# Optimization experiments

Hardware: AMD Instinct MI355X
Metric: run time of the kernel (lower is better)

The kernel has to match this reference:

```python
import jax, jax.numpy as jnp
import numpy as np

# ActivationWithGain: activation scaled so a standard-normal input keeps unit variance.
_s = np.random.default_rng(0).standard_normal(1 << 20).astype(np.float32)
GAIN = float(1.0 / (_s / (1.0 + np.exp(-_s))).std())  # SiLU gain ~ 1.787
INV_SQRT2 = np.float32(1.0 / np.sqrt(2.0))


def _act(x):
    return jax.nn.silu(x) * jnp.float32(GAIN)


def setup_inputs() -> dict:
    key = jax.random.key(0)
    ks = jax.random.split(key, 9)
    n_up, n_dn, n_nuc, dim, edim = 512, 512, 256, 256, 32
    n_el = n_up + n_dn
    n_edges = n_el * n_nuc  # dense electron-nucleus bipartite graph
    return {
        "elec_emb": jax.random.normal(ks[0], (n_el, dim), jnp.float32),
        "up_inp": jax.random.normal(ks[1], (n_nuc, dim), jnp.float32),
        "down_inp": jax.random.normal(ks[2], (n_nuc, dim), jnp.float32),
        "edge_emb": jax.random.normal(ks[3], (n_edges, edim), jnp.float32),
        "contr": jax.random.uniform(ks[4], (n_edges,), jnp.float32),
        "norm": jax.random.uniform(ks[5], (n_el,), jnp.float32),
        "W_out": jax.random.normal(ks[6], (dim, dim), jnp.float32) / np.float32(np.sqrt(dim)),
        "b_out": jnp.zeros((dim,), jnp.float32),
        "W_edge": jax.random.normal(ks[7], (edim, dim), jnp.float32) / np.float32(np.sqrt(edim)),
        "W_out2": jax.random.normal(ks[8], (dim, dim), jnp.float32) / np.float32(np.sqrt(dim)),
        "b_out2": jnp.zeros((dim,), jnp.float32),
        "scale1": jnp.ones((), jnp.float32),  # FixedScalingFactor (frozen after init)
        "scale2": jnp.ones((), jnp.float32),
        "n_up": n_up,
        "n_down": n_dn,
        "n_nuclei": n_nuc,
    }


def reference(elec_emb, up_inp, down_inp, edge_emb, contr, norm,
              W_out, b_out, W_edge, W_out2, b_out2, scale1, scale2,
              n_up, n_down, n_nuclei):
    n_el = n_up + n_down
    # adj_idx for a single graph: dense bipartite edges, sorted by electron index
    e_n_i = jnp.repeat(jnp.arange(n_el), n_nuclei)   # [E] electron index per edge
    e_n_k = jnp.tile(jnp.arange(n_nuclei), n_el)     # [E] nucleus index per edge

    out_emb = elec_emb @ W_out + b_out               # Dense(out_dim)

    mask = jnp.arange(n_el) < n_up                   # spin_mask: True for spin-up electrons
    e_n_mask = mask[e_n_i]
    # gather nuclear embeddings per edge, selecting up/down table by electron spin
    inp = jnp.where(e_n_mask[:, None], up_inp[e_n_k], down_inp[e_n_k])  # [E, D]

    weights = edge_emb @ W_edge                      # Dense_no_bias(out_dim), [E, D]
    # FixedScalingFactor: contr only weights the init-time variance estimate;
    # at runtime the op is x * scale1.
    to_elec = inp * weights * scale1                 # [E, D]

    agg = jax.ops.segment_sum(to_elec, e_n_i, num_segments=n_el,
                              indices_are_sorted=True)  # [n_el, D]
    out_emb = (out_emb + agg * norm[:, None]) * scale2
    out_emb = _act(out_emb)
    out_emb = _act(out_emb @ W_out2 + b_out2)
    # residual: shapes match, so rescaled sum
    return (elec_emb + out_emb) * INV_SQRT2
```

## Files before the change

kernel.cpp:

```cpp
#include <hip/hip_runtime.h>
#include <hip/hip_bf16.h>

#define N_EL   1024
#define N_UP   512
#define NNUC   256
#define DIM    256
#define EDIM   32
#define KTOT   8192
#define NKP    16

#define GAIN_F      1.7872135f
#define INV_SQRT2_F 0.7071067811865476f

typedef __attribute__((ext_vector_type(8))) short bf16x8;
typedef __attribute__((ext_vector_type(4))) short bf16x4;
typedef __attribute__((ext_vector_type(4))) float f32x4;

__device__ __forceinline__ short f2bf(float x) {
    union { __hip_bfloat16 h; short s; } u;
    u.h = __float2bfloat16(x);
    return u.s;
}

__global__ __launch_bounds__(256) void prep_kernel(
    const float* __restrict__ up, const float* __restrict__ dn,
    const float* __restrict__ wedge,
    const float* __restrict__ w1, const float* __restrict__ w2,
    const float* __restrict__ elec,
    short* __restrict__ w1f, short* __restrict__ w2f,
    short* __restrict__ elecb, short* __restrict__ Tf)
{
    const int idx = (blockIdx.x << 8) + threadIdx.x;

    if (idx < 65536) {
        {
            const int b  = idx & 7;
            const int l  = (idx >> 3) & 63;
            const int q  = (idx >> 9) & 7;
            const int nt = idx >> 12;
            const int j  = (q << 5) + ((l >> 4) << 3) + b;
            const int d  = (nt << 4) + (l & 15);
            w1f[idx] = f2bf(w1[j * DIM + d]);
            w2f[idx] = f2bf(w2[j * DIM + d]);
        }
        {
            const f32x4 v = *(const f32x4*)(elec + (idx << 2));
            bf16x4 o;
            o[0] = f2bf(v[0]); o[1] = f2bf(v[1]);
            o[2] = f2bf(v[2]); o[3] = f2bf(v[3]);
            *(bf16x4*)(elecb + (idx << 2)) = o;
        }
    }

    {
        const int s   = idx >> 18;
        const int rem = idx & 262143;
        const int kt  = rem >> 10;
        const int dt  = (rem >> 6) & 15;
        const int l   = rem & 63;
        const int d   = (dt << 4) + (l & 15);
        const int jb  = (l >> 4) << 3;
        const float* __restrict__ inp = s ? dn : up;
        const float iv = inp[kt * DIM + d];
        const float* __restrict__ wcol = wedge + d;
        bf16x8 o;
        #pragma unroll
        for (int b = 0; b < 8; ++b)
            o[b] = f2bf(iv * wcol[(jb + b) * DIM]);
        *(bf16x8*)(Tf + ((size_t)s << 21) + ((size_t)rem << 3)) = o;
    }
}

__global__ __launch_bounds__(512) void edge_gemm(
    const float* __restrict__ eemb,
    const short* __restrict__ Tf,
    float* __restrict__ P)
{
    __shared__ short A_lds[2][4096];

    const int tid  = threadIdx.x;
    const int w    = tid >> 6;
    const int lane = tid & 63;
    const int g    = lane >> 4;
    const int c    = lane & 15;
    const int kp   = blockIdx.x & 15;
    const int rt   = blockIdx.x >> 4;
    const int rb   = rt << 5;
    const int kb   = kp << 9;

    const short* __restrict__ Tb = Tf + ((rb < N_UP) ? 0 : (1 << 21));

    const int f  = w;
    const int r_ = f >> 2;
    const int q_ = f & 3;
    const float* __restrict__ Asrc = eemb
        + (size_t)(rb + (r_ << 4) + c) * KTOT
        + kb + (q_ << 5) + (g << 3);

    f32x4 s_lo, s_hi;
    bf16x8 bA[8], bB[8];

    auto STAGE_LOAD = [&](int sub) {
        const float* p = Asrc + (sub << 7);
        s_lo = *(const f32x4*)p;
        s_hi = *(const f32x4*)(p + 4);
    };
    auto STAGE_WRITE = [&](int buf) {
        union { bf16x8 v; short s[8]; } o;
        o.s[0] = f2bf(s_lo[0]); o.s[1] = f2bf(s_lo[1]);
        o.s[2] = f2bf(s_lo[2]); o.s[3] = f2bf(s_lo[3]);
        o.s[4] = f2bf(s_hi[0]); o.s[5] = f2bf(s_hi[1]);
        o.s[6] = f2bf(s_hi[2]); o.s[7] = f2bf(s_hi[3]);
        *(bf16x8*)(&A_lds[buf][(f << 9) + (lane << 3)]) = o.v;
    };
    auto LOADB = [&](int sub, bf16x8 (&bd)[8]) {
        #pragma unroll
        for (int t = 0; t < 2; ++t) {
            const int ct = (w << 1) + t;
            #pragma unroll
            for (int q = 0; q < 4; ++q) {
                const int ktg = (kp << 4) + (sub << 2) + q;
                bd[(t << 2) + q] = *(const bf16x8*)(
                    Tb + (((((ktg << 4) + ct) << 6) + lane) << 3));
            }
        }
    };

    f32x4 acc[2][2] = {{{0.f,0.f,0.f,0.f},{0.f,0.f,0.f,0.f}},
                       {{0.f,0.f,0.f,0.f},{0.f,0.f,0.f,0.f}}};

    auto COMPUTE = [&](int buf, bf16x8 (&bc)[8]) {
        bf16x8 a[2][4];
        #pragma unroll
        for (int rr = 0; rr < 2; ++rr)
            #pragma unroll
            for (int q = 0; q < 4; ++q)
                a[rr][q] = *(const bf16x8*)(
                    &A_lds[buf][((((rr << 2) + q)) << 9) + (lane << 3)]);
        #pragma unroll
        for (int q = 0; q < 4; ++q) {
            acc[0][0] = __builtin_amdgcn_mfma_f32_16x16x32_bf16(a[0][q], bc[q],     acc[0][0], 0, 0, 0);
            acc[0][1] = __builtin_amdgcn_mfma_f32_16x16x32_bf16(a[0][q], bc[4 + q], acc[0][1], 0, 0, 0);
            acc[1][0] = __builtin_amdgcn_mfma_f32_16x16x32_bf16(a[1][q], bc[q],     acc[1][0], 0, 0, 0);
            acc[1][1] = __builtin_amdgcn_mfma_f32_16x16x32_bf16(a[1][q], bc[4 + q], acc[1][1], 0, 0, 0);
        }
    };

    STAGE_LOAD(0);
    LOADB(0, bA);
    STAGE_WRITE(0);
    __syncthreads();

    #pragma unroll
    for (int sub = 0; sub < 4; ++sub) {
        if ((sub & 1) == 0) {
            if (sub < 3) { STAGE_LOAD(sub + 1); LOADB(sub + 1, bB); }
            COMPUTE(0, bA);
        } else {
            if (sub < 3) { STAGE_LOAD(sub + 1); LOADB(sub + 1, bA); }
            COMPUTE(1, bB);
        }
        if (sub < 3) STAGE_WRITE((sub & 1) ^ 1);
        __syncthreads();
    }

    float* __restrict__ Pp = P + ((size_t)kp << 18);
    #pragma unroll
    for (int rr = 0; rr < 2; ++rr)
        #pragma unroll
        for (int t = 0; t < 2; ++t) {
            const int ct = (w << 1) + t;
            #pragma unroll
            for (int j = 0; j < 4; ++j) {
                const int row = rb + (rr << 4) + (g << 2) + j;
                Pp[(row << 8) + (ct << 4) + c] = acc[rr][t][j];
            }
        }
}

__global__ __launch_bounds__(256) void reduce_kernel(
    const float* __restrict__ P,
    const float* __restrict__ s1p,
    float* __restrict__ agg)
{
    const int idx = (blockIdx.x << 8) + threadIdx.x;
    const float s1 = *s1p;
    f32x4 s = {0.f, 0.f, 0.f, 0.f};
    #pragma unroll
    for (int kp = 0; kp < NKP; ++kp) {
        const f32x4 v = *(const f32x4*)(P + ((size_t)kp << 18) + (idx << 2));
        s[0] += v[0]; s[1] += v[1]; s[2] += v[2]; s[3] += v[3];
    }
    s[0] *= s1; s[1] *= s1; s[2] *= s1; s[3] *= s1;
    *(f32x4*)(agg + (idx << 2)) = s;
}

__global__ __launch_bounds__(512) void out_kernel(
    const short* __restrict__ elecb,
    const short* __restrict__ w1f, const short* __restrict__ w2f,
    const float* __restrict__ elec, const float* __restrict__ agg,
    const float* __restrict__ norm,
    const float* __restrict__ b1, const float* __restrict__ b2,
    const float* __restrict__ s2p,
    float* __restrict__ outp)
{
    __shared__ short h_s[16][264];

    const int tid  = threadIdx.x;
    const int w    = tid >> 6;
    const int lane = tid & 63;
    const int g    = lane >> 4;
    const int c    = lane & 15;
    const int mt   = blockIdx.x >> 2;
    const int qd   = blockIdx.x & 3;
    const int mb   = mt << 4;

    const short* abase = elecb + ((mb + c) << 8) + (g << 3);
    bf16x8 a[8];
    #pragma unroll
    for (int q = 0; q < 8; ++q) a[q] = *(const bf16x8*)(abase + (q << 5));

    const float s2 = *s2p;

    #pragma unroll
    for (int t = 0; t < 2; ++t) {
        const int ct = (w << 1) + t;
        const short* bb = w1f + (ct << 12) + (lane << 3);
        bf16x8 b[8];
        #pragma unroll
        for (int q = 0; q < 8; ++q) b[q] = *(const bf16x8*)(bb + (q << 9));
        f32x4 acc = {0.f, 0.f, 0.f, 0.f};
        #pragma unroll
        for (int q = 0; q < 8; ++q)
            acc = __builtin_amdgcn_mfma_f32_16x16x32_bf16(a[q], b[q], acc, 0, 0, 0);

        const int n  = (ct << 4) + c;
        const float bv = b1[n];
        #pragma unroll
        for (int r = 0; r < 4; ++r) {
            const int mr = (g << 2) + r;
            const int m  = mb + mr;
            const float y = (acc[r] + bv + agg[(m << 8) + n] * norm[m]) * s2;
            const float sig = 1.f / (1.f + __expf(-y));
            h_s[mr][n] = f2bf(GAIN_F * y * sig);
        }
    }
    __syncthreads();

    if (w < 4) {
        bf16x8 a2[8];
        #pragma unroll
        for (int q = 0; q < 8; ++q)
            a2[q] = *(const bf16x8*)(&h_s[c][(q << 5) + (g << 3)]);

        const int ct = (qd << 2) + w;
        const short* bb = w2f + (ct << 12) + (lane << 3);
        bf16x8 b[8];
        #pragma unroll
        for (int q = 0; q < 8; ++q) b[q] = *(const bf16x8*)(bb + (q << 9));
        f32x4 acc = {0.f, 0.f, 0.f, 0.f};
        #pragma unroll
        for (int q = 0; q < 8; ++q)
            acc = __builtin_amdgcn_mfma_f32_16x16x32_bf16(a2[q], b[q], acc, 0, 0, 0);

        const int n  = (ct << 4) + c;
        const float bv = b2[n];
        #pragma unroll
        for (int r = 0; r < 4; ++r) {
            const int m = mb + (g << 2) + r;
            const float z = acc[r] + bv;
            const float sig = 1.f / (1.f + __expf(-z));
            const float o = GAIN_F * z * sig;
            outp[(m << 8) + n] = (elec[(m << 8) + n] + o) * INV_SQRT2_F;
        }
    }
}

extern "C" void kernel_launch(void* const* d_in, const int* in_sizes, int n_in,
                              void* d_out, int out_size, void* d_ws, size_t ws_size,
                              hipStream_t stream)
{
    const float* elec  = (const float*)d_in[0];
    const float* up    = (const float*)d_in[1];
    const float* dn    = (const float*)d_in[2];
    const float* eemb  = (const float*)d_in[3];
    const float* norm  = (const float*)d_in[5];
    const float* W1    = (const float*)d_in[6];
    const float* b1    = (const float*)d_in[7];
    const float* Wedge = (const float*)d_in[8];
    const float* W2    = (const float*)d_in[9];
    const float* b2    = (const float*)d_in[10];
    const float* s1    = (const float*)d_in[11];
    const float* s2    = (const float*)d_in[12];

    short* sbase = (short*)d_ws;
    short* w1f   = sbase;
    short* w2f   = sbase + 65536;
    short* elecb = sbase + 131072;
    short* Tf    = sbase + 393216;
    float* P     = (float*)(sbase + 393216 + 4194304);
    float* agg   = P + (size_t)NKP * 262144;

    prep_kernel  <<<2048, 256, 0, stream>>>(up, dn, Wedge, W1, W2, elec,
                                            w1f, w2f, elecb, Tf);
    edge_gemm    <<<512, 512, 0, stream>>>(eemb, Tf, P);
    reduce_kernel<<<256, 256, 0, stream>>>(P, s1, agg);
    out_kernel   <<<256, 512, 0, stream>>>(elecb, w1f, w2f, elec, agg, norm,
                                           b1, b2, s2, (float*)d_out);
}
```

Measured before the change: 32.79 us.

## Load edge-embedding A fragments directly from global, drop LDS staging and barriers

The edge GEMM no longer stages the fp32 edge-embedding tile through double-buffered shared memory. Each wave now loads its own A fragments straight from global memory, converts them to bf16 in registers and feeds the MFMAs, with no __syncthreads. This removes the LDS round trip and the block-wide barriers. In exchange, all 8 waves redundantly load the same A data (8x more global/L2 traffic), and the explicit software prefetch that overlapped the next loads with compute is lost.

After: 55.22 us. +68.4%, slower.

```diff
diff --git a/kernel.cpp b/kernel.cpp
--- a/kernel.cpp
+++ b/kernel.cpp
@@ -76,8 +76,6 @@
     const short* __restrict__ Tf,
     float* __restrict__ P)
 {
-    __shared__ short A_lds[2][4096];
-
     const int tid  = threadIdx.x;
     const int w    = tid >> 6;
     const int lane = tid & 63;
@@ -90,78 +88,48 @@
 
     const short* __restrict__ Tb = Tf + ((rb < N_UP) ? 0 : (1 << 21));
 
-    const int f  = w;
-    const int r_ = f >> 2;
-    const int q_ = f & 3;
-    const float* __restrict__ Asrc = eemb
-        + (size_t)(rb + (r_ << 4) + c) * KTOT
-        + kb + (q_ << 5) + (g << 3);
-
-    f32x4 s_lo, s_hi;
-    bf16x8 bA[8], bB[8];
-
-    auto STAGE_LOAD = [&](int sub) {
-        const float* p = Asrc + (sub << 7);
-        s_lo = *(const f32x4*)p;
-        s_hi = *(const f32x4*)(p + 4);
-    };
-    auto STAGE_WRITE = [&](int buf) {
-        union { bf16x8 v; short s[8]; } o;
-        o.s[0] = f2bf(s_lo[0]); o.s[1] = f2bf(s_lo[1]);
-        o.s[2] = f2bf(s_lo[2]); o.s[3] = f2bf(s_lo[3]);
-        o.s[4] = f2bf(s_hi[0]); o.s[5] = f2bf(s_hi[1]);
-        o.s[6] = f2bf(s_hi[2]); o.s[7] = f2bf(s_hi[3]);
-        *(bf16x8*)(&A_lds[buf][(f << 9) + (lane << 3)]) = o.v;
-    };
-    auto LOADB = [&](int sub, bf16x8 (&bd)[8]) {
+    const float* __restrict__ Arow0 = eemb + (size_t)(rb + c) * KTOT + kb + (g << 3);
+    const float* __restrict__ Arow1 = Arow0 + (size_t)16 * KTOT;
+
+    f32x4 acc[2][2] = {{{0.f,0.f,0.f,0.f},{0.f,0.f,0.f,0.f}},
+                       {{0.f,0.f,0.f,0.f},{0.f,0.f,0.f,0.f}}};
+
+    #pragma unroll
+    for (int sub = 0; sub < 4; ++sub) {
+        bf16x8 a[2][4];
+        #pragma unroll
+        for (int rr = 0; rr < 2; ++rr) {
+            const float* base = (rr ? Arow1 : Arow0) + (sub << 7);
+            #pragma unroll
+            for (int q = 0; q < 4; ++q) {
+                const f32x4 lo = *(const f32x4*)(base + (q << 5));
+                const f32x4 hi = *(const f32x4*)(base + (q << 5) + 4);
+                union { bf16x8 v; short s[8]; } f;
+                f.s[0] = f2bf(lo[0]); f.s[1] = f2bf(lo[1]);
+                f.s[2] = f2bf(lo[2]); f.s[3] = f2bf(lo[3]);
+                f.s[4] = f2bf(hi[0]); f.s[5] = f2bf(hi[1]);
+                f.s[6] = f2bf(hi[2]); f.s[7] = f2bf(hi[3]);
+                a[rr][q] = f.v;
+            }
+        }
+        bf16x8 b[8];
         #pragma unroll
         for (int t = 0; t < 2; ++t) {
             const int ct = (w << 1) + t;
             #pragma unroll
             for (int q = 0; q < 4; ++q) {
                 const int ktg = (kp << 4) + (sub << 2) + q;
-                bd[(t << 2) + q] = *(const bf16x8*)(
+                b[(t << 2) + q] = *(const bf16x8*)(
                     Tb + (((((ktg << 4) + ct) << 6) + lane) << 3));
             }
         }
-    };
-
-    f32x4 acc[2][2] = {{{0.f,0.f,0.f,0.f},{0.f,0.f,0.f,0.f}},
-                       {{0.f,0.f,0.f,0.f},{0.f,0.f,0.f,0.f}}};
-
-    auto COMPUTE = [&](int buf, bf16x8 (&bc)[8]) {
-        bf16x8 a[2][4];
-        #pragma unroll
-        for (int rr = 0; rr < 2; ++rr)
-            #pragma unroll
-            for (int q = 0; q < 4; ++q)
-                a[rr][q] = *(const bf16x8*)(
-                    &A_lds[buf][((((rr << 2) + q)) << 9) + (lane << 3)]);
         #pragma unroll
         for (int q = 0; q < 4; ++q) {
-            acc[0][0] = __builtin_amdgcn_mfma_f32_16x16x32_bf16(a[0][q], bc[q],     acc[0][0], 0, 0, 0);
-            acc[0][1] = __builtin_amdgcn_mfma_f32_16x16x32_bf16(a[0][q], bc[4 + q], acc[0][1], 0, 0, 0);
-            acc[1][0] = __builtin_amdgcn_mfma_f32_16x16x32_bf16(a[1][q], bc[q],     acc[1][0], 0, 0, 0);
-            acc[1][1] = __builtin_amdgcn_mfma_f32_16x16x32_bf16(a[1][q], bc[4 + q], acc[1][1], 0, 0, 0);
-        }
-    };
-
-    STAGE_LOAD(0);
-    LOADB(0, bA);
-    STAGE_WRITE(0);
-    __syncthreads();
-
-    #pragma unroll
-    for (int sub = 0; sub < 4; ++sub) {
-        if ((sub & 1) == 0) {
-            if (sub < 3) { STAGE_LOAD(sub + 1); LOADB(sub + 1, bB); }
-            COMPUTE(0, bA);
-        } else {
-            if (sub < 3) { STAGE_LOAD(sub + 1); LOADB(sub + 1, bA); }
-            COMPUTE(1, bB);
-        }
-        if (sub < 3) STAGE_WRITE((sub & 1) ^ 1);
-        __syncthreads();
+            acc[0][0] = __builtin_amdgcn_mfma_f32_16x16x32_bf16(a[0][q], b[q],     acc[0][0], 0, 0, 0);
+            acc[0][1] = __builtin_amdgcn_mfma_f32_16x16x32_bf16(a[0][q], b[4 + q], acc[0][1], 0, 0, 0);
+            acc[1][0] = __builtin_amdgcn_mfma_f32_16x16x32_bf16(a[1][q], b[q],     acc[1][0], 0, 0, 0);
+            acc[1][1] = __builtin_amdgcn_mfma_f32_16x16x32_bf16(a[1][q], b[4 + q], acc[1][1], 0, 0, 0);
+        }
     }
 
     float* __restrict__ Pp = P + ((size_t)kp << 18);
```
